# Optimization experiments

Measured on AMD Instinct MI355X. Metric: run time of the kernel, lower is better.

Reference implementation:

```python
import jax, jax.numpy as jnp
import numpy as np


def _grid_sample_bilinear_zeros(img, grid):
    # img: (B, C, H, W); grid: (B, Nq, P, 2) in [-1, 1], align_corners=False,
    # padding_mode='zeros' (matches torch.nn.functional.grid_sample).
    B, C, H, W = img.shape
    gx, gy = grid[..., 0], grid[..., 1]
    x = ((gx + 1.0) * W - 1.0) * 0.5  # pixel coords
    y = ((gy + 1.0) * H - 1.0) * 0.5
    x0 = jnp.floor(x)
    y0 = jnp.floor(y)
    wx1 = x - x0
    wx0 = 1.0 - wx1
    wy1 = y - y0
    wy0 = 1.0 - wy1
    imgf = img.reshape(B, C, H * W)

    def gather(ix, iy):
        ixi = ix.astype(jnp.int32)
        iyi = iy.astype(jnp.int32)
        valid = (ixi >= 0) & (ixi < W) & (iyi >= 0) & (iyi < H)  # (B,Nq,P)
        lin = jnp.clip(iyi, 0, H - 1) * W + jnp.clip(ixi, 0, W - 1)
        v = jnp.take_along_axis(imgf, lin.reshape(B, 1, -1), axis=2)
        v = v.reshape(B, C, lin.shape[1], lin.shape[2])  # (B,C,Nq,P)
        return v * valid[:, None, :, :].astype(img.dtype)

    out = (gather(x0, y0) * (wx0 * wy0)[:, None]
           + gather(x0 + 1.0, y0) * (wx1 * wy0)[:, None]
           + gather(x0, y0 + 1.0) * (wx0 * wy1)[:, None]
           + gather(x0 + 1.0, y0 + 1.0) * (wx1 * wy1)[:, None])
    return out  # (B, C, Nq, P)


def setup_inputs() -> dict:
    key = jax.random.key(0)
    k1, k2, k3, k4 = jax.random.split(key, 4)
    B, H, W, C, P = 4, 128, 128, 128, 4
    N = H * W
    x = jax.random.normal(k1, (B, N, C), dtype=jnp.float32)
    deltaA = jax.random.normal(k2, (B, N, C), dtype=jnp.float32)
    # sampling_offsets Linear(d_model -> n_points*2): weight (2P, C), bias (2P,)
    Wo = jax.random.normal(k3, (2 * P, C), dtype=jnp.float32) * 0.02
    bo = jax.random.normal(k4, (2 * P,), dtype=jnp.float32)
    return {"x": x, "deltaA": deltaA, "H": H, "W": W, "Wo": Wo, "bo": bo}


def reference(x, deltaA, H, W, Wo, bo):
    B, N, C = x.shape
    P = Wo.shape[0] // 2
    # reference points for a single level (valid_ratios == 1), points_type == 0
    ry = (jnp.arange(H, dtype=x.dtype) + 0.5) / H
    rx = (jnp.arange(W, dtype=x.dtype) + 0.5) / W
    gy, gx = jnp.meshgrid(ry, rx, indexing="ij")  # (H, W)
    ref = jnp.stack([gx.reshape(-1), gy.reshape(-1)], axis=-1)  # (N, 2) as (x, y)
    # learned offsets, normalized by (W, H)
    off = (jnp.einsum("bnc,oc->bno", x, Wo) + bo).reshape(B, N, P, 2)
    norm = jnp.array([W, H], dtype=x.dtype)
    loc = ref[None, :, None, :] + off / norm  # (B, N, P, 2) in [0,1]
    grid = 2.0 * loc - 1.0
    # value = concat(x, deltaA) laid out as (B, 2C, H, W)
    val = jnp.concatenate([x, deltaA], axis=-1)  # (B, N, 2C)
    img = jnp.swapaxes(val, 1, 2).reshape(B, 2 * C, H, W)
    samp = _grid_sample_bilinear_zeros(img, grid)  # (B, 2C, N, P)
    feat, wt = samp[:, :C], samp[:, C:]
    agg = feat * (wt - jnp.swapaxes(deltaA, 1, 2)[..., None])  # (B, C, N, P)
    out = jnp.swapaxes(agg.mean(axis=-1), 1, 2)  # (B, N, C)
    sampling_locations = loc.reshape(B, N, 1, 1, P, 2)
    return out, sampling_locations
```

## Files before the change

kernel.cpp:

```cpp
#include <hip/hip_runtime.h>


#define HW_ 128
#define CC_ 128
#define PP_ 4
#define NN_ (HW_ * HW_)

typedef float f32x4 __attribute__((ext_vector_type(4)));
typedef _Float16 f16x8 __attribute__((ext_vector_type(8)));

__global__ __launch_bounds__(256) void sao_pack(
    const float* __restrict__ x,
    const float* __restrict__ dA,
    const float* __restrict__ Wo,
    const float* __restrict__ bo,
    float* __restrict__ locs,
    _Float16* __restrict__ packed)
{
    const int lane = threadIdx.x & 63;
    const int h = lane >> 5;
    const int s = lane & 31;
    const int wv = threadIdx.x >> 6;
    const int pt = blockIdx.x * 8 + wv * 2 + h;
    const size_t rowstart = (size_t)pt * CC_;

    const float4 xo = *(const float4*)(x + rowstart + s * 4);
    const float4 dd = *(const float4*)(dA + rowstart + s * 4);

    float4 wf[8];
#pragma unroll
    for (int o = 0; o < 8; ++o)
        wf[o] = *(const float4*)(Wo + o * CC_ + s * 4);

    f16x8 pk;
    pk[0] = (_Float16)xo.x; pk[1] = (_Float16)xo.y;
    pk[2] = (_Float16)xo.z; pk[3] = (_Float16)xo.w;
    pk[4] = (_Float16)dd.x; pk[5] = (_Float16)dd.y;
    pk[6] = (_Float16)dd.z; pk[7] = (_Float16)dd.w;
    *(f16x8*)(packed + (size_t)pt * 256 + s * 8) = pk;

    float p[8];
#pragma unroll
    for (int o = 0; o < 8; ++o)
        p[o] = xo.x * wf[o].x + xo.y * wf[o].y + xo.z * wf[o].z + xo.w * wf[o].w;

#pragma unroll
    for (int m = 1; m <= 16; m <<= 1) {
#pragma unroll
        for (int o = 0; o < 8; ++o)
            p[o] += __shfl_xor(p[o], m);
    }

    if (s < 8) {
        float off = 0.0f;
#pragma unroll
        for (int o = 0; o < 8; ++o)
            if (o == s) off = p[o];
        off += bo[s];
        const int n = pt & (NN_ - 1);
        const int ix = n & (HW_ - 1);
        const int iy = n >> 7;
        const float refx = (ix + 0.5f) * (1.0f / HW_);
        const float refy = (iy + 0.5f) * (1.0f / HW_);
        const float ref = (s & 1) ? refy : refx;
        locs[(size_t)pt * 8 + s] = ref + off * (1.0f / HW_);
    }
}

__global__ __launch_bounds__(256) void sao_gather(
    const _Float16* __restrict__ packed,
    const float* __restrict__ locs,
    float* __restrict__ out)
{
    const int lane = threadIdx.x & 63;
    const int h = lane >> 5;
    const int s = lane & 31;
    const int wv = threadIdx.x >> 6;

    const int nblk = gridDim.x;
    const int q = nblk >> 3, r = nblk & 7;
    const int xcd = blockIdx.x & 7;
    const int work = (xcd < r ? xcd * (q + 1) : r * (q + 1) + (xcd - r) * q)
                     + (blockIdx.x >> 3);

    const int pt = work * 8 + wv * 2 + h;
    const int b = pt >> 14;
    const size_t rowstart = (size_t)pt * CC_;

    const f32x4 lo0 = *(const f32x4*)(locs + (size_t)pt * 8);
    const f32x4 lo1 = *(const f32x4*)(locs + (size_t)pt * 8 + 4);
    const float lx[4] = {lo0.x, lo0.z, lo1.x, lo1.z};
    const float ly[4] = {lo0.y, lo0.w, lo1.y, lo1.w};

    const f16x8 own = *(const f16x8*)(packed + (size_t)pt * 256 + s * 8);

    int eoff[PP_][4];
    float wgt[PP_][4];
#pragma unroll
    for (int p = 0; p < PP_; ++p) {
        const float gx = 2.0f * lx[p] - 1.0f;
        const float gy = 2.0f * ly[p] - 1.0f;
        const float xp = ((gx + 1.0f) * (float)HW_ - 1.0f) * 0.5f;
        const float yp = ((gy + 1.0f) * (float)HW_ - 1.0f) * 0.5f;
        const float x0f = floorf(xp), y0f = floorf(yp);
        const float wx1 = xp - x0f, wy1 = yp - y0f;
        const float wx0 = 1.0f - wx1, wy0 = 1.0f - wy1;
        const int ix0 = (int)x0f, iy0 = (int)y0f;
#pragma unroll
        for (int k = 0; k < 4; ++k) {
            const int cx = ix0 + (k & 1);
            const int cy = iy0 + (k >> 1);
            const bool valid = (cx >= 0) & (cx < HW_) & (cy >= 0) & (cy < HW_);
            float w = ((k & 1) ? wx1 : wx0) * ((k >> 1) ? wy1 : wy0);
            wgt[p][k] = valid ? w : 0.0f;
            const int pix = min(max(cy, 0), HW_ - 1) * HW_ + min(max(cx, 0), HW_ - 1);
            eoff[p][k] = pix * 256;
        }
    }

    const _Float16* pb = packed + (size_t)b * ((size_t)NN_ * 256) + s * 8;

    f16x8 fw[PP_];
#pragma unroll
    for (int p = 0; p < PP_; ++p) {
        f16x8 a0 = *(const f16x8*)(pb + eoff[p][0]);
        f16x8 a1 = *(const f16x8*)(pb + eoff[p][1]);
        f16x8 a2 = *(const f16x8*)(pb + eoff[p][2]);
        f16x8 a3 = *(const f16x8*)(pb + eoff[p][3]);
        fw[p] = a0 * (_Float16)wgt[p][0] + a1 * (_Float16)wgt[p][1]
              + a2 * (_Float16)wgt[p][2] + a3 * (_Float16)wgt[p][3];
    }

    f32x4 acc;
    acc.x = acc.y = acc.z = acc.w = 0.0f;
    const float d0 = (float)own[4], d1 = (float)own[5];
    const float d2 = (float)own[6], d3 = (float)own[7];
#pragma unroll
    for (int p = 0; p < PP_; ++p) {
        acc.x = fmaf((float)fw[p][0], (float)fw[p][4] - d0, acc.x);
        acc.y = fmaf((float)fw[p][1], (float)fw[p][5] - d1, acc.y);
        acc.z = fmaf((float)fw[p][2], (float)fw[p][6] - d2, acc.z);
        acc.w = fmaf((float)fw[p][3], (float)fw[p][7] - d3, acc.w);
    }

    f32x4 res;
    res.x = acc.x * 0.25f;
    res.y = acc.y * 0.25f;
    res.z = acc.z * 0.25f;
    res.w = acc.w * 0.25f;
    __builtin_nontemporal_store(res, (f32x4*)(out + rowstart + s * 4));
}

__global__ __launch_bounds__(256) void sao_fused(
    const float* __restrict__ x,
    const float* __restrict__ dA,
    const float* __restrict__ Wo,
    const float* __restrict__ bo,
    float* __restrict__ out,
    float* __restrict__ locs)
{
    const int lane = threadIdx.x & 63;
    const int h = lane >> 5;
    const int s = lane & 31;
    const int wv = threadIdx.x >> 6;
    const int nblk = gridDim.x;
    const int q = nblk >> 3, r = nblk & 7;
    const int xcd = blockIdx.x & 7;
    const int work = (xcd < r ? xcd * (q + 1) : r * (q + 1) + (xcd - r) * q)
                     + (blockIdx.x >> 3);
    const int pt = work * 8 + wv * 2 + h;
    const int b = pt >> 14;
    const int n = pt & (NN_ - 1);
    const int ix = n & (HW_ - 1);
    const int iy = n >> 7;
    const size_t rowstart = (size_t)pt * CC_;
    const float4 d4 = *(const float4*)(dA + rowstart + s * 4);
    const int o = s & 7;
    const int chunk = s >> 3;
    const float* xr = x + rowstart + chunk * 32;
    const float* wr = Wo + o * CC_ + chunk * 32;
    float partial = 0.0f;
#pragma unroll
    for (int j = 0; j < 8; ++j) {
        const float4 xv = *(const float4*)(xr + 4 * j);
        const float4 wvv = *(const float4*)(wr + 4 * j);
        partial += xv.x * wvv.x + xv.y * wvv.y + xv.z * wvv.z + xv.w * wvv.w;
    }
    partial += __shfl_xor(partial, 8);
    partial += __shfl_xor(partial, 16);
    const float offv = partial + bo[o];
    const float refx = (ix + 0.5f) * (1.0f / HW_);
    const float refy = (iy + 0.5f) * (1.0f / HW_);
    if (s < 8) {
        const float ref = (o & 1) ? refy : refx;
        locs[(size_t)pt * 8 + o] = ref + offv * (1.0f / HW_);
    }
    float offs[8];
#pragma unroll
    for (int oo = 0; oo < 8; ++oo)
        offs[oo] = __shfl(offv, oo, 32);
    const size_t bbase = (size_t)b * (size_t)(NN_ * CC_) + s * 4;
    float4 acc = make_float4(0.f, 0.f, 0.f, 0.f);
#pragma unroll
    for (int p = 0; p < PP_; ++p) {
        const float locx = refx + offs[2 * p] * (1.0f / HW_);
        const float locy = refy + offs[2 * p + 1] * (1.0f / HW_);
        const float gx = 2.0f * locx - 1.0f;
        const float gy = 2.0f * locy - 1.0f;
        const float xp = ((gx + 1.0f) * (float)HW_ - 1.0f) * 0.5f;
        const float yp = ((gy + 1.0f) * (float)HW_ - 1.0f) * 0.5f;
        const float x0f = floorf(xp), y0f = floorf(yp);
        const float wx1 = xp - x0f, wy1 = yp - y0f;
        const float wx0 = 1.0f - wx1, wy0 = 1.0f - wy1;
        const int ix0 = (int)x0f, iy0 = (int)y0f;
        float4 feat = make_float4(0.f, 0.f, 0.f, 0.f);
        float4 wt = make_float4(0.f, 0.f, 0.f, 0.f);
#pragma unroll
        for (int k = 0; k < 4; ++k) {
            const int cx = ix0 + (k & 1);
            const int cy = iy0 + (k >> 1);
            const bool valid = (cx >= 0) & (cx < HW_) & (cy >= 0) & (cy < HW_);
            float w = ((k & 1) ? wx1 : wx0) * ((k >> 1) ? wy1 : wy0);
            w = valid ? w : 0.0f;
            const int pix = min(max(cy, 0), HW_ - 1) * HW_ + min(max(cx, 0), HW_ - 1);
            const size_t cb = bbase + (size_t)pix * CC_;
            const float4 xv = *(const float4*)(x + cb);
            const float4 dv = *(const float4*)(dA + cb);
            feat.x = fmaf(w, xv.x, feat.x);
            feat.y = fmaf(w, xv.y, feat.y);
            feat.z = fmaf(w, xv.z, feat.z);
            feat.w = fmaf(w, xv.w, feat.w);
            wt.x = fmaf(w, dv.x, wt.x);
            wt.y = fmaf(w, dv.y, wt.y);
            wt.z = fmaf(w, dv.z, wt.z);
            wt.w = fmaf(w, dv.w, wt.w);
        }
        acc.x = fmaf(feat.x, wt.x - d4.x, acc.x);
        acc.y = fmaf(feat.y, wt.y - d4.y, acc.y);
        acc.z = fmaf(feat.z, wt.z - d4.z, acc.z);
        acc.w = fmaf(feat.w, wt.w - d4.w, acc.w);
    }
    f32x4 res;
    res.x = acc.x * 0.25f;
    res.y = acc.y * 0.25f;
    res.z = acc.z * 0.25f;
    res.w = acc.w * 0.25f;
    __builtin_nontemporal_store(res, (f32x4*)(out + rowstart + s * 4));
}

extern "C" void kernel_launch(void* const* d_in, const int* in_sizes, int n_in,
                              void* d_out, int out_size, void* d_ws, size_t ws_size,
                              hipStream_t stream) {
    const float* x = (const float*)d_in[0];
    const float* dA = (const float*)d_in[1];
    const float* Wo = (const float*)d_in[4];
    const float* bo = (const float*)d_in[5];
    float* out = (float*)d_out;

    const int points = in_sizes[0] / CC_;
    float* locs = out + (size_t)points * CC_;
    const int blocks = points / 8;

    const size_t need = (size_t)points * 256 * sizeof(_Float16);
    if (ws_size >= need) {
        _Float16* packed = (_Float16*)d_ws;
        sao_pack<<<blocks, 256, 0, stream>>>(x, dA, Wo, bo, locs, packed);
        sao_gather<<<blocks, 256, 0, stream>>>(packed, locs, out);
    } else {
        sao_fused<<<blocks, 256, 0, stream>>>(x, dA, Wo, bo, out, locs);
    }
}
```

Before: 46.34 us.

## Swizzle pack blocks across XCDs, use a butterfly reduction, batch gather loads

The pack kernel now uses the same XCD-aware block-to-work mapping as the gather kernel, so each XCD produces the rows it later reads from its own L2. Its input loads become nontemporal. The 8-output shuffle reduction is replaced by a recursive-halving butterfly that drops the shuffle count from 40 to about 9 and leaves each lane holding its own output. In the gather kernel, all 16 neighbor loads are issued before any arithmetic to raise memory-level parallelism, at the cost of higher register pressure.

```diff
diff --git a/kernel.cpp b/kernel.cpp
--- a/kernel.cpp
+++ b/kernel.cpp
@@ -8,6 +8,12 @@
 
 typedef float f32x4 __attribute__((ext_vector_type(4)));
 typedef _Float16 f16x8 __attribute__((ext_vector_type(8)));
+
+__device__ __forceinline__ int swizzled_work(int blk, int nblk) {
+    const int q = nblk >> 3, r = nblk & 7;
+    const int xcd = blk & 7;
+    return (xcd < r ? xcd * (q + 1) : r * (q + 1) + (xcd - r) * q) + (blk >> 3);
+}
 
 __global__ __launch_bounds__(256) void sao_pack(
     const float* __restrict__ x,
@@ -21,11 +27,12 @@
     const int h = lane >> 5;
     const int s = lane & 31;
     const int wv = threadIdx.x >> 6;
-    const int pt = blockIdx.x * 8 + wv * 2 + h;
+    const int work = swizzled_work(blockIdx.x, gridDim.x);
+    const int pt = work * 8 + wv * 2 + h;
     const size_t rowstart = (size_t)pt * CC_;
 
-    const float4 xo = *(const float4*)(x + rowstart + s * 4);
-    const float4 dd = *(const float4*)(dA + rowstart + s * 4);
+    const f32x4 xo = __builtin_nontemporal_load((const f32x4*)(x + rowstart + s * 4));
+    const f32x4 dd = __builtin_nontemporal_load((const f32x4*)(dA + rowstart + s * 4));
 
     float4 wf[8];
 #pragma unroll
@@ -44,19 +51,33 @@
     for (int o = 0; o < 8; ++o)
         p[o] = xo.x * wf[o].x + xo.y * wf[o].y + xo.z * wf[o].z + xo.w * wf[o].w;
 
-#pragma unroll
-    for (int m = 1; m <= 16; m <<= 1) {
-#pragma unroll
-        for (int o = 0; o < 8; ++o)
-            p[o] += __shfl_xor(p[o], m);
-    }
+    const int t0 = s & 1;
+    float q4[4];
+#pragma unroll
+    for (int j = 0; j < 4; ++j) {
+        const float keep = t0 ? p[2 * j + 1] : p[2 * j];
+        const float send = t0 ? p[2 * j] : p[2 * j + 1];
+        q4[j] = keep + __shfl_xor(send, 1);
+    }
+    const int t1 = (s >> 1) & 1;
+    float r2[2];
+#pragma unroll
+    for (int i = 0; i < 2; ++i) {
+        const float keep = t1 ? q4[2 * i + 1] : q4[2 * i];
+        const float send = t1 ? q4[2 * i] : q4[2 * i + 1];
+        r2[i] = keep + __shfl_xor(send, 2);
+    }
+    const int t2 = (s >> 2) & 1;
+    {
+        const float keep = t2 ? r2[1] : r2[0];
+        const float send = t2 ? r2[0] : r2[1];
+        r2[0] = keep + __shfl_xor(send, 4);
+    }
+    r2[0] += __shfl_xor(r2[0], 8);
+    r2[0] += __shfl_xor(r2[0], 16);
 
     if (s < 8) {
-        float off = 0.0f;
-#pragma unroll
-        for (int o = 0; o < 8; ++o)
-            if (o == s) off = p[o];
-        off += bo[s];
+        const float off = r2[0] + bo[s];
         const int n = pt & (NN_ - 1);
         const int ix = n & (HW_ - 1);
         const int iy = n >> 7;
@@ -76,13 +97,7 @@
     const int h = lane >> 5;
     const int s = lane & 31;
     const int wv = threadIdx.x >> 6;
-
-    const int nblk = gridDim.x;
-    const int q = nblk >> 3, r = nblk & 7;
-    const int xcd = blockIdx.x & 7;
-    const int work = (xcd < r ? xcd * (q + 1) : r * (q + 1) + (xcd - r) * q)
-                     + (blockIdx.x >> 3);
-
+    const int work = swizzled_work(blockIdx.x, gridDim.x);
     const int pt = work * 8 + wv * 2 + h;
     const int b = pt >> 14;
     const size_t rowstart = (size_t)pt * CC_;
@@ -120,15 +135,20 @@
 
     const _Float16* pb = packed + (size_t)b * ((size_t)NN_ * 256) + s * 8;
 
+    f16x8 g[16];
+#pragma unroll
+    for (int p = 0; p < PP_; ++p)
+#pragma unroll
+        for (int k = 0; k < 4; ++k)
+            g[p * 4 + k] = *(const f16x8*)(pb + eoff[p][k]);
+
     f16x8 fw[PP_];
 #pragma unroll
     for (int p = 0; p < PP_; ++p) {
-        f16x8 a0 = *(const f16x8*)(pb + eoff[p][0]);
-        f16x8 a1 = *(const f16x8*)(pb + eoff[p][1]);
-        f16x8 a2 = *(const f16x8*)(pb + eoff[p][2]);
-        f16x8 a3 = *(const f16x8*)(pb + eoff[p][3]);
-        fw[p] = a0 * (_Float16)wgt[p][0] + a1 * (_Float16)wgt[p][1]
-              + a2 * (_Float16)wgt[p][2] + a3 * (_Float16)wgt[p][3];
+        fw[p] = g[p * 4 + 0] * (_Float16)wgt[p][0]
+              + g[p * 4 + 1] * (_Float16)wgt[p][1]
+              + g[p * 4 + 2] * (_Float16)wgt[p][2]
+              + g[p * 4 + 3] * (_Float16)wgt[p][3];
     }
 
     f32x4 acc;
@@ -163,11 +183,7 @@
     const int h = lane >> 5;
     const int s = lane & 31;
     const int wv = threadIdx.x >> 6;
-    const int nblk = gridDim.x;
-    const int q = nblk >> 3, r = nblk & 7;
-    const int xcd = blockIdx.x & 7;
-    const int work = (xcd < r ? xcd * (q + 1) : r * (q + 1) + (xcd - r) * q)
-                     + (blockIdx.x >> 3);
+    const int work = swizzled_work(blockIdx.x, gridDim.x);
     const int pt = work * 8 + wv * 2 + h;
     const int b = pt >> 14;
     const int n = pt & (NN_ - 1);
```

Result: slower. 48.85 us (+5.4%).
